# Kernel optimization log

Measured on AMD Instinct MI355X. Metric: run time of the kernel, lower is better.

Reference implementation:

```python
import jax, jax.numpy as jnp
import numpy as np

B, L_DEC, L_ENC = 4, 1024, 1024
D_MODEL, D_INNER, N_HEAD, D_K, D_V = 512, 256, 8, 64, 64
TEMP = D_K ** 0.5
EPS = 1e-6


def _layernorm(x, g, b):
    mu = jnp.mean(x, axis=-1, keepdims=True)
    var = jnp.mean(jnp.square(x - mu), axis=-1, keepdims=True)
    return (x - mu) * jax.lax.rsqrt(var + EPS) * g + b


def _mha(x_q, x_kv, Wq, Wk, Wv, Wfc, ln_g, ln_b, mask):
    # Faithful to source: only the query input is layer-normed; k/v use raw x_kv.
    resid = x_q
    qn = _layernorm(x_q, ln_g, ln_b)
    # Stacked per-head projections: Wq/Wk/Wv are [H, d_k, d_model]
    q = jnp.einsum('bld,hkd->bhlk', qn, Wq) / TEMP   # [B,H,Lq,dk]
    k = jnp.einsum('bld,hkd->bhlk', x_kv, Wk)        # [B,H,Lk,dk]
    v = jnp.einsum('bld,hkd->bhlk', x_kv, Wv)        # [B,H,Lk,dv]
    scores = jnp.einsum('bhqd,bhkd->bhqk', q, k)     # [B,H,Lq,Lk]
    if mask is not None:
        scores = jnp.where(mask[:, None, :, :] == 0, -jnp.inf, scores)
    attn = jax.nn.softmax(scores, axis=-1)
    out = jnp.einsum('bhqk,bhkd->bhqd', attn, v)     # [B,H,Lq,dv]
    Bq, H, Lq, dv = out.shape
    out = out.transpose(0, 2, 1, 3).reshape(Bq, Lq, H * dv)
    return out @ Wfc.T + resid


def _ffn(x, W1, b1, W2, b2, ln_g, ln_b):
    resid = x
    h = _layernorm(x, ln_g, ln_b)
    h = jax.nn.relu(h @ W1.T + b1) @ W2.T + b2
    return h + resid


def setup_inputs() -> dict:
    key = jax.random.key(0)
    ks = jax.random.split(key, 20)
    s = 0.02
    dec_input = jax.random.normal(ks[0], (B, L_DEC, D_MODEL), jnp.float32)
    enc_output = jax.random.normal(ks[1], (B, L_ENC, D_MODEL), jnp.float32)
    slf_attn_mask = jnp.tril(jnp.ones((1, L_DEC, L_DEC), jnp.int32))  # causal
    p = {}
    for i, pre in enumerate(['slf', 'enc']):
        base = 2 + i * 4
        p[f'{pre}_Wq'] = jax.random.normal(ks[base], (N_HEAD, D_K, D_MODEL), jnp.float32) * s
        p[f'{pre}_Wk'] = jax.random.normal(ks[base + 1], (N_HEAD, D_K, D_MODEL), jnp.float32) * s
        p[f'{pre}_Wv'] = jax.random.normal(ks[base + 2], (N_HEAD, D_V, D_MODEL), jnp.float32) * s
        p[f'{pre}_Wfc'] = jax.random.normal(ks[base + 3], (D_MODEL, N_HEAD * D_V), jnp.float32) * s
        p[f'{pre}_ln_g'] = jnp.ones((D_MODEL,), jnp.float32)
        p[f'{pre}_ln_b'] = jnp.zeros((D_MODEL,), jnp.float32)
    p['ffn_W1'] = jax.random.normal(ks[10], (D_INNER, D_MODEL), jnp.float32) * s
    p['ffn_b1'] = jnp.zeros((D_INNER,), jnp.float32)
    p['ffn_W2'] = jax.random.normal(ks[11], (D_MODEL, D_INNER), jnp.float32) * s
    p['ffn_b2'] = jnp.zeros((D_MODEL,), jnp.float32)
    p['ffn_ln_g'] = jnp.ones((D_MODEL,), jnp.float32)
    p['ffn_ln_b'] = jnp.zeros((D_MODEL,), jnp.float32)
    return {'dec_input': dec_input, 'enc_output': enc_output,
            'slf_attn_mask': slf_attn_mask, **p}


def reference(dec_input, enc_output,
              slf_Wq, slf_Wk, slf_Wv, slf_Wfc, slf_ln_g, slf_ln_b,
              enc_Wq, enc_Wk, enc_Wv, enc_Wfc, enc_ln_g, enc_ln_b,
              ffn_W1, ffn_b1, ffn_W2, ffn_b2, ffn_ln_g, ffn_ln_b,
              slf_attn_mask):
    x = _mha(dec_input, dec_input, slf_Wq, slf_Wk, slf_Wv, slf_Wfc,
             slf_ln_g, slf_ln_b, slf_attn_mask)
    x = _mha(x, enc_output, enc_Wq, enc_Wk, enc_Wv, enc_Wfc,
             enc_ln_g, enc_ln_b, None)
    x = _ffn(x, ffn_W1, ffn_b1, ffn_W2, ffn_b2, ffn_ln_g, ffn_ln_b)
    return x
```

## Files before the change

kernel.cpp:

```cpp
#include <hip/hip_runtime.h>
#include <hip/hip_bf16.h>
#include <math.h>

#define DMODEL 512
#define NHEAD  8
#define DHEAD  64

typedef __attribute__((ext_vector_type(8))) short bf16x8;
typedef __attribute__((ext_vector_type(4))) float f32x4;
typedef __attribute__((ext_vector_type(4))) short short4v;

static __device__ inline short f2bf(float f) {
    __hip_bfloat16 h = __float2bfloat16(f);
    return *reinterpret_cast<short*>(&h);
}

#define GLOAD_LDS16(gp, lp)                                                      \
    __builtin_amdgcn_global_load_lds(                                            \
        (const __attribute__((address_space(1))) unsigned int*)(gp),             \
        (__attribute__((address_space(3))) unsigned int*)(lp), 16, 0, 0)

struct PrepArgs {
    const float* src[10];
    short*       dst[10];
    int          n[10];
    const float* X;
    const float* gam;
    const float* bet;
    short*       Y;
    short*       Xd;
    const float* E;
    short*       Ed;
    int          ln_blocks;
};

__global__ __launch_bounds__(256) void prep_kernel(PrepArgs a) {
    const int bx = blockIdx.x;
    if (bx < a.ln_blocks) {
        int row = bx * 4 + (threadIdx.x >> 6);
        int tid = threadIdx.x & 63;
        const float* x = a.X + (size_t)row * DMODEL;
        float4 v0 = *(const float4*)(x + tid * 4);
        float4 v1 = *(const float4*)(x + 256 + tid * 4);
        float sum = v0.x + v0.y + v0.z + v0.w + v1.x + v1.y + v1.z + v1.w;
        float sq  = v0.x*v0.x + v0.y*v0.y + v0.z*v0.z + v0.w*v0.w
                  + v1.x*v1.x + v1.y*v1.y + v1.z*v1.z + v1.w*v1.w;
#pragma unroll
        for (int off = 1; off < 64; off <<= 1) {
            sum += __shfl_xor(sum, off);
            sq  += __shfl_xor(sq, off);
        }
        float mu  = sum * (1.0f / DMODEL);
        float var = sq * (1.0f / DMODEL) - mu * mu;
        float r   = rsqrtf(var + 1e-6f);
        float4 g1 = *(const float4*)(a.gam + tid * 4);
        float4 c1 = *(const float4*)(a.bet + tid * 4);
        float4 g2 = *(const float4*)(a.gam + 256 + tid * 4);
        float4 c2 = *(const float4*)(a.bet + 256 + tid * 4);
        short4v y1, y2;
        y1.x = f2bf((v0.x - mu) * r * g1.x + c1.x);
        y1.y = f2bf((v0.y - mu) * r * g1.y + c1.y);
        y1.z = f2bf((v0.z - mu) * r * g1.z + c1.z);
        y1.w = f2bf((v0.w - mu) * r * g1.w + c1.w);
        y2.x = f2bf((v1.x - mu) * r * g2.x + c2.x);
        y2.y = f2bf((v1.y - mu) * r * g2.y + c2.y);
        y2.z = f2bf((v1.z - mu) * r * g2.z + c2.z);
        y2.w = f2bf((v1.w - mu) * r * g2.w + c2.w);
        short* y = a.Y + (size_t)row * DMODEL;
        *(short4v*)(y + tid * 4)       = y1;
        *(short4v*)(y + 256 + tid * 4) = y2;
        short4v d1, d2;
        d1.x = f2bf(v0.x); d1.y = f2bf(v0.y); d1.z = f2bf(v0.z); d1.w = f2bf(v0.w);
        d2.x = f2bf(v1.x); d2.y = f2bf(v1.y); d2.z = f2bf(v1.z); d2.w = f2bf(v1.w);
        short* d = a.Xd + (size_t)row * DMODEL;
        *(short4v*)(d + tid * 4)       = d1;
        *(short4v*)(d + 256 + tid * 4) = d2;
        const float* e = a.E + (size_t)row * DMODEL;
        float4 ea = *(const float4*)(e + tid * 4);
        float4 eb = *(const float4*)(e + 256 + tid * 4);
        short4v e1, e2;
        e1.x = f2bf(ea.x); e1.y = f2bf(ea.y); e1.z = f2bf(ea.z); e1.w = f2bf(ea.w);
        e2.x = f2bf(eb.x); e2.y = f2bf(eb.y); e2.z = f2bf(eb.z); e2.w = f2bf(eb.w);
        short* ed = a.Ed + (size_t)row * DMODEL;
        *(short4v*)(ed + tid * 4)       = e1;
        *(short4v*)(ed + 256 + tid * 4) = e2;
    } else {
        int cb = bx - a.ln_blocks;
        int t = cb >> 7;
        int idx = ((cb & 127) * 256 + threadIdx.x) * 8;
        if (idx >= a.n[t]) return;
        const float* s = a.src[t] + idx;
        float4 p = *(const float4*)s;
        float4 q = *(const float4*)(s + 4);
        bf16x8 o;
        o[0] = f2bf(p.x); o[1] = f2bf(p.y); o[2] = f2bf(p.z); o[3] = f2bf(p.w);
        o[4] = f2bf(q.x); o[5] = f2bf(q.y); o[6] = f2bf(q.z); o[7] = f2bf(q.w);
        *(bf16x8*)(a.dst[t] + idx) = o;
    }
}

__global__ __launch_bounds__(256) void ln_kernel(const float* __restrict__ X,
                                                 const float* __restrict__ gam,
                                                 const float* __restrict__ bet,
                                                 short* __restrict__ Y) {
    int row = blockIdx.x * 4 + (threadIdx.x >> 6);
    int tid = threadIdx.x & 63;
    const float* x = X + (size_t)row * DMODEL;
    float4 a = *(const float4*)(x + tid * 4);
    float4 b = *(const float4*)(x + 256 + tid * 4);
    float sum = a.x + a.y + a.z + a.w + b.x + b.y + b.z + b.w;
    float sq  = a.x*a.x + a.y*a.y + a.z*a.z + a.w*a.w
              + b.x*b.x + b.y*b.y + b.z*b.z + b.w*b.w;
#pragma unroll
    for (int off = 1; off < 64; off <<= 1) {
        sum += __shfl_xor(sum, off);
        sq  += __shfl_xor(sq, off);
    }
    float mu  = sum * (1.0f / DMODEL);
    float var = sq * (1.0f / DMODEL) - mu * mu;
    float r   = rsqrtf(var + 1e-6f);
    float4 g1 = *(const float4*)(gam + tid * 4);
    float4 c1 = *(const float4*)(bet + tid * 4);
    float4 g2 = *(const float4*)(gam + 256 + tid * 4);
    float4 c2 = *(const float4*)(bet + 256 + tid * 4);
    short4v y1, y2;
    y1.x = f2bf((a.x - mu) * r * g1.x + c1.x);
    y1.y = f2bf((a.y - mu) * r * g1.y + c1.y);
    y1.z = f2bf((a.z - mu) * r * g1.z + c1.z);
    y1.w = f2bf((a.w - mu) * r * g1.w + c1.w);
    y2.x = f2bf((b.x - mu) * r * g2.x + c2.x);
    y2.y = f2bf((b.y - mu) * r * g2.y + c2.y);
    y2.z = f2bf((b.z - mu) * r * g2.z + c2.z);
    y2.w = f2bf((b.w - mu) * r * g2.w + c2.w);
    short* y = Y + (size_t)row * DMODEL;
    *(short4v*)(y + tid * 4)       = y1;
    *(short4v*)(y + 256 + tid * 4) = y2;
}

struct GJobs {
    const short* A[3];
    const short* W[3];
    const float* bias[3];
    const float* resid[3];
    void*        C[3];
    int M[3], N[3], K[3];
    float scale[3];
    int relu[3], obf[3], nblk[3];
};

__global__ __launch_bounds__(256) void gemm_bf16(GJobs jb) {
    __shared__ short As[2][64 * 64];
    __shared__ short Bs[2][64 * 64];

    int bid = blockIdx.x, j = 0;
    while (j < 2 && bid >= jb.nblk[j]) { bid -= jb.nblk[j]; ++j; }
    const short* __restrict__ A = jb.A[j];
    const short* __restrict__ W = jb.W[j];
    const int N = jb.N[j], K = jb.K[j];
    const int nbx = N >> 6;
    const int tn = (bid % nbx) * 64;
    const int tm = (bid / nbx) * 64;

    const int tid  = threadIdx.x;
    const int w    = tid >> 6;
    const int l    = tid & 63;
    const int lq   = l & 15;
    const int g    = l >> 4;
    const int wm   = (w >> 1) * 32;
    const int wn   = (w & 1) * 32;
    const int lrow = l >> 3;
    const int lsl  = l & 7;

    f32x4 acc[2][2];
#pragma unroll
    for (int i = 0; i < 2; ++i)
#pragma unroll
        for (int jj = 0; jj < 2; ++jj)
            acc[i][jj] = (f32x4){0.f, 0.f, 0.f, 0.f};

#define GSTAGE(buf, koff)                                                        \
    do {                                                                         \
        _Pragma("unroll")                                                        \
        for (int i_ = 0; i_ < 2; ++i_) {                                         \
            int row_ = i_ * 32 + w * 8 + lrow;                                   \
            int slot_ = lsl ^ (row_ & 7);                                        \
            GLOAD_LDS16(A + (size_t)(tm + row_) * K + (koff) + slot_ * 8,        \
                        As[buf] + i_ * 2048 + w * 512);                          \
            GLOAD_LDS16(W + (size_t)(tn + row_) * K + (koff) + slot_ * 8,        \
                        Bs[buf] + i_ * 2048 + w * 512);                          \
        }                                                                        \
    } while (0)

    GSTAGE(0, 0);
    int buf = 0;
#pragma unroll 1
    for (int k0 = 0; k0 < K; k0 += 64, buf ^= 1) {
        __syncthreads();
        if (k0 + 64 < K) GSTAGE(buf ^ 1, k0 + 64);
#pragma unroll
        for (int ks = 0; ks < 2; ++ks) {
            const int sl = ((ks * 4 + g) ^ (lq & 7)) * 8;
            bf16x8 af[2], bfv[2];
#pragma unroll
            for (int i = 0; i < 2; ++i) {
                af[i]  = *(const bf16x8*)&As[buf][(wm + i * 16 + lq) * 64 + sl];
                bfv[i] = *(const bf16x8*)&Bs[buf][(wn + i * 16 + lq) * 64 + sl];
            }
#pragma unroll
            for (int i = 0; i < 2; ++i)
#pragma unroll
                for (int jj = 0; jj < 2; ++jj)
                    acc[i][jj] = __builtin_amdgcn_mfma_f32_16x16x32_bf16(
                        af[i], bfv[jj], acc[i][jj], 0, 0, 0);
        }
    }
#undef GSTAGE

    const float* bias  = jb.bias[j];
    const float* resid = jb.resid[j];
    const float scale  = jb.scale[j];
    const int relu = jb.relu[j], obf = jb.obf[j];
#pragma unroll
    for (int i = 0; i < 2; ++i) {
#pragma unroll
        for (int r = 0; r < 4; ++r) {
            int row = tm + wm + i * 16 + g * 4 + r;
#pragma unroll
            for (int jj = 0; jj < 2; ++jj) {
                int col = tn + wn + jj * 16 + lq;
                float v = acc[i][jj][r] * scale;
                if (bias)  v += bias[col];
                if (resid) v += resid[(size_t)row * N + col];
                if (relu)  v = fmaxf(v, 0.f);
                if (obf) ((short*)jb.C[j])[(size_t)row * N + col] = f2bf(v);
                else     ((float*)jb.C[j])[(size_t)row * N + col] = v;
            }
        }
    }
}

__global__ __launch_bounds__(256) void attn_mfma_kernel(
        const short* __restrict__ Q, const short* __restrict__ K,
        const short* __restrict__ V, short* __restrict__ O,
        int Lq, int Lk, int causal, int qs, int kvs) {
    __shared__ short Kt[2][64 * 64];
    __shared__ short Vt[2][64][72];
    __shared__ short Pb[4][16][72];

    const int tid  = threadIdx.x;
    const int wave = tid >> 6;
    const int lane = tid & 63;
    const int lq   = lane & 15;
    const int g    = lane >> 4;
    const int bh   = blockIdx.y;
    const int b = bh >> 3, h = bh & 7;
    const int band = causal ? ((bh < 16) ? (int)blockIdx.x : (15 - (int)blockIdx.x))
                            : (int)blockIdx.x;
    const int qt = band * 4 + wave;
    const int q0 = qt * 16;
    const float NEG = -__builtin_inff();

    size_t qoff = (size_t)(b * Lq + q0 + lq) * qs + h * DHEAD;
    bf16x8 qf0 = *(const bf16x8*)(Q + qoff + g * 8);
    bf16x8 qf1 = *(const bf16x8*)(Q + qoff + 32 + g * 8);

    f32x4 o[4] = {{0,0,0,0},{0,0,0,0},{0,0,0,0},{0,0,0,0}};
    f32x4 lacc = {0.f, 0.f, 0.f, 0.f};

    bf16x8 ones;
    {
        short ov = (lq == 0) ? (short)0x3F80 : (short)0;
#pragma unroll
        for (int i = 0; i < 8; ++i) ones[i] = ov;
    }

    const int nkt = causal ? (band + 1) : (Lk >> 6);
    const int lrow = lane >> 3;
    const int lsl  = lane & 7;
    const int va = tid & 31;
    const int vd = (tid >> 5) * 8;

    bf16x8 vr0, vr1;
    auto stageK = [&](int kt, int bf) {
#pragma unroll
        for (int i = 0; i < 2; ++i) {
            int row = i * 32 + wave * 8 + lrow;
            int slot = lsl ^ (row & 7);
            GLOAD_LDS16(K + (size_t)(b * Lk + kt * 64 + row) * kvs + h * DHEAD + slot * 8,
                        Kt[bf] + i * 2048 + wave * 512);
        }
    };
    auto loadV = [&](int kt) {
        size_t gb = (size_t)(b * Lk + kt * 64 + 2 * va) * kvs + h * DHEAD + vd;
        vr0 = *(const bf16x8*)(V + gb);
        vr1 = *(const bf16x8*)(V + gb + kvs);
    };
    auto writeV = [&](int bf) {
#pragma unroll
        for (int i = 0; i < 8; ++i) {
            unsigned p = (unsigned short)vr0[i] | ((unsigned)(unsigned short)vr1[i] << 16);
            *(unsigned*)&Vt[bf][vd + i][2 * va] = p;
        }
    };

    stageK(0, 0);
    loadV(0);
    writeV(0);
    __syncthreads();

#pragma unroll 1
    for (int kt = 0; kt < nkt; ++kt) {
        const int cur = kt & 1;
        if (kt + 1 < nkt) { stageK(kt + 1, cur ^ 1); loadV(kt + 1); }

        f32x4 s[4];
#pragma unroll
        for (int sub = 0; sub < 4; ++sub) {
            int rr = sub * 16 + lq;
            const int sl0 = ((0 + g) ^ (lq & 7)) * 8;
            const int sl1 = ((4 + g) ^ (lq & 7)) * 8;
            bf16x8 kf0 = *(const bf16x8*)&Kt[cur][rr * 64 + sl0];
            bf16x8 kf1 = *(const bf16x8*)&Kt[cur][rr * 64 + sl1];
            f32x4 a = {0.f, 0.f, 0.f, 0.f};
            a = __builtin_amdgcn_mfma_f32_16x16x32_bf16(kf0, qf0, a, 0, 0, 0);
            a = __builtin_amdgcn_mfma_f32_16x16x32_bf16(kf1, qf1, a, 0, 0, 0);
            s[sub] = a;
        }
        if (causal && kt == nkt - 1) {
            int qg = q0 + lq;
#pragma unroll
            for (int sub = 0; sub < 4; ++sub) {
#pragma unroll
                for (int r = 0; r < 4; ++r) {
                    int kg = kt * 64 + sub * 16 + g * 4 + r;
                    if (kg > qg) s[sub][r] = NEG;
                }
            }
        }

#pragma unroll
        for (int sub = 0; sub < 4; ++sub) {
            short4v p4;
            p4.x = f2bf(exp2f(fminf(s[sub][0], 85.f)));
            p4.y = f2bf(exp2f(fminf(s[sub][1], 85.f)));
            p4.z = f2bf(exp2f(fminf(s[sub][2], 85.f)));
            p4.w = f2bf(exp2f(fminf(s[sub][3], 85.f)));
            *(short4v*)&Pb[wave][lq][sub * 16 + g * 4] = p4;
        }
        bf16x8 pf0 = *(const bf16x8*)&Pb[wave][lq][g * 8];
        bf16x8 pf1 = *(const bf16x8*)&Pb[wave][lq][32 + g * 8];

#pragma unroll
        for (int dc = 0; dc < 4; ++dc) {
            bf16x8 vf0 = *(const bf16x8*)&Vt[cur][dc * 16 + lq][g * 8];
            bf16x8 vf1 = *(const bf16x8*)&Vt[cur][dc * 16 + lq][32 + g * 8];
            o[dc] = __builtin_amdgcn_mfma_f32_16x16x32_bf16(pf0, vf0, o[dc], 0, 0, 0);
            o[dc] = __builtin_amdgcn_mfma_f32_16x16x32_bf16(pf1, vf1, o[dc], 0, 0, 0);
        }
        lacc = __builtin_amdgcn_mfma_f32_16x16x32_bf16(pf0, ones, lacc, 0, 0, 0);
        lacc = __builtin_amdgcn_mfma_f32_16x16x32_bf16(pf1, ones, lacc, 0, 0, 0);

        if (kt + 1 < nkt) writeV(cur ^ 1);
        __syncthreads();
    }

#pragma unroll
    for (int r = 0; r < 4; ++r) {
        float lr = __shfl(lacc[r], g << 4);
        float inv = 1.f / lr;
        size_t ob = (size_t)(b * Lq + q0 + g * 4 + r) * qs + h * DHEAD + lq;
        O[ob + 0]  = f2bf(o[0][r] * inv);
        O[ob + 16] = f2bf(o[1][r] * inv);
        O[ob + 32] = f2bf(o[2][r] * inv);
        O[ob + 48] = f2bf(o[3][r] * inv);
    }
}

static void launch_gemm(GJobs& jb, int njobs, hipStream_t stream) {
    int total = 0;
    for (int i = 0; i < 3; ++i) { if (i >= njobs) jb.nblk[i] = 0; total += jb.nblk[i]; }
    gemm_bf16<<<total, 256, 0, stream>>>(jb);
}

extern "C" void kernel_launch(void* const* d_in, const int* in_sizes, int n_in,
                              void* d_out, int out_size, void* d_ws, size_t ws_size,
                              hipStream_t stream) {
    const float* dec       = (const float*)d_in[0];
    const float* enc       = (const float*)d_in[1];
    const float* slf_Wq    = (const float*)d_in[3];
    const float* slf_Wk    = (const float*)d_in[4];
    const float* slf_Wv    = (const float*)d_in[5];
    const float* slf_Wfc   = (const float*)d_in[6];
    const float* slf_ln_g  = (const float*)d_in[7];
    const float* slf_ln_b  = (const float*)d_in[8];
    const float* enc_Wq    = (const float*)d_in[9];
    const float* enc_Wk    = (const float*)d_in[10];
    const float* enc_Wv    = (const float*)d_in[11];
    const float* enc_Wfc   = (const float*)d_in[12];
    const float* enc_ln_g  = (const float*)d_in[13];
    const float* enc_ln_b  = (const float*)d_in[14];
    const float* ffn_W1    = (const float*)d_in[15];
    const float* ffn_b1    = (const float*)d_in[16];
    const float* ffn_W2    = (const float*)d_in[17];
    const float* ffn_b2    = (const float*)d_in[18];
    const float* ffn_ln_g  = (const float*)d_in[19];
    const float* ffn_ln_b  = (const float*)d_in[20];
    float* out = (float*)d_out;

    const int Bb = 4, L = 1024, M = Bb * L;
    const size_t NE = (size_t)M * DMODEL;
    const int WQN = NHEAD * DHEAD * DMODEL;
    const float QSCALE = 0.125f * 1.44269504f;
    float* ws = (float*)d_ws;
    float* x1 = ws;
    float* x2 = ws + NE;
    short* kv16e = (short*)x2;
    short* sb = (short*)(ws + 2 * NE);
    short* dec16 = sb;               sb += NE;
    short* enc16 = sb;               sb += NE;
    short* qn16  = sb;               sb += NE;
    short* q16   = sb;               sb += NE;
    short* ao16  = sb;               sb += NE;
    short* kv16  = sb;               sb += 2 * NE;
    short* h16   = sb;               sb += NE / 2;
    short* wq_s  = sb;               sb += WQN;
    short* wkv_s = sb;               sb += 2 * WQN;
    short* wfc_s = sb;               sb += WQN;
    short* wq_e  = sb;               sb += WQN;
    short* wkv_e = sb;               sb += 2 * WQN;
    short* wfc_e = sb;               sb += WQN;
    short* w1_16 = sb;               sb += 256 * DMODEL;
    short* w2_16 = sb;               sb += DMODEL * 256;

    PrepArgs pa;
    pa.src[0] = slf_Wq;  pa.dst[0] = wq_s;          pa.n[0] = WQN;
    pa.src[1] = slf_Wk;  pa.dst[1] = wkv_s;         pa.n[1] = WQN;
    pa.src[2] = slf_Wv;  pa.dst[2] = wkv_s + WQN;   pa.n[2] = WQN;
    pa.src[3] = slf_Wfc; pa.dst[3] = wfc_s;         pa.n[3] = WQN;
    pa.src[4] = enc_Wq;  pa.dst[4] = wq_e;          pa.n[4] = WQN;
    pa.src[5] = enc_Wk;  pa.dst[5] = wkv_e;         pa.n[5] = WQN;
    pa.src[6] = enc_Wv;  pa.dst[6] = wkv_e + WQN;   pa.n[6] = WQN;
    pa.src[7] = enc_Wfc; pa.dst[7] = wfc_e;         pa.n[7] = WQN;
    pa.src[8] = ffn_W1;  pa.dst[8] = w1_16;         pa.n[8] = 256 * DMODEL;
    pa.src[9] = ffn_W2;  pa.dst[9] = w2_16;         pa.n[9] = DMODEL * 256;
    pa.X = dec; pa.gam = slf_ln_g; pa.bet = slf_ln_b; pa.Y = qn16;
    pa.Xd = dec16; pa.E = enc; pa.Ed = enc16;
    pa.ln_blocks = M / 4;
    prep_kernel<<<M / 4 + 10 * 128, 256, 0, stream>>>(pa);

    dim3 attn_grid(L / 64, Bb * NHEAD);
    const int NB512  = (M / 64) * (512 / 64);
    const int NB1024 = (M / 64) * (1024 / 64);
    const int NB256  = (M / 64) * (256 / 64);

    {
        GJobs jb = {};
        jb.A[0] = qn16;  jb.W[0] = wq_s;  jb.C[0] = q16;
        jb.M[0] = M; jb.N[0] = 512;  jb.K[0] = 512; jb.scale[0] = QSCALE;
        jb.obf[0] = 1; jb.nblk[0] = NB512;
        jb.A[1] = dec16; jb.W[1] = wkv_s; jb.C[1] = kv16;
        jb.M[1] = M; jb.N[1] = 1024; jb.K[1] = 512; jb.scale[1] = 1.f;
        jb.obf[1] = 1; jb.nblk[1] = NB1024;
        jb.A[2] = enc16; jb.W[2] = wkv_e; jb.C[2] = kv16e;
        jb.M[2] = M; jb.N[2] = 1024; jb.K[2] = 512; jb.scale[2] = 1.f;
        jb.obf[2] = 1; jb.nblk[2] = NB1024;
        launch_gemm(jb, 3, stream);
    }
    attn_mfma_kernel<<<attn_grid, 256, 0, stream>>>(q16, kv16, kv16 + 512, ao16,
                                                    L, L, 1, DMODEL, 1024);
    {
        GJobs jb = {};
        jb.A[0] = ao16; jb.W[0] = wfc_s; jb.resid[0] = dec; jb.C[0] = x1;
        jb.M[0] = M; jb.N[0] = 512; jb.K[0] = 512; jb.scale[0] = 1.f;
        jb.obf[0] = 0; jb.nblk[0] = NB512;
        launch_gemm(jb, 1, stream);
    }

    ln_kernel<<<M / 4, 256, 0, stream>>>(x1, enc_ln_g, enc_ln_b, qn16);
    {
        GJobs jb = {};
        jb.A[0] = qn16; jb.W[0] = wq_e; jb.C[0] = q16;
        jb.M[0] = M; jb.N[0] = 512; jb.K[0] = 512; jb.scale[0] = QSCALE;
        jb.obf[0] = 1; jb.nblk[0] = NB512;
        launch_gemm(jb, 1, stream);
    }
    attn_mfma_kernel<<<attn_grid, 256, 0, stream>>>(q16, kv16e, kv16e + 512, ao16,
                                                    L, L, 0, DMODEL, 1024);
    {
        GJobs jb = {};
        jb.A[0] = ao16; jb.W[0] = wfc_e; jb.resid[0] = x1; jb.C[0] = x2;
        jb.M[0] = M; jb.N[0] = 512; jb.K[0] = 512; jb.scale[0] = 1.f;
        jb.obf[0] = 0; jb.nblk[0] = NB512;
        launch_gemm(jb, 1, stream);
    }

    ln_kernel<<<M / 4, 256, 0, stream>>>(x2, ffn_ln_g, ffn_ln_b, qn16);
    {
        GJobs jb = {};
        jb.A[0] = qn16; jb.W[0] = w1_16; jb.bias[0] = ffn_b1; jb.C[0] = h16;
        jb.M[0] = M; jb.N[0] = 256; jb.K[0] = 512; jb.scale[0] = 1.f;
        jb.relu[0] = 1; jb.obf[0] = 1; jb.nblk[0] = NB256;
        launch_gemm(jb, 1, stream);
    }
    {
        GJobs jb = {};
        jb.A[0] = h16; jb.W[0] = w2_16; jb.bias[0] = ffn_b2; jb.resid[0] = x2;
        jb.C[0] = out;
        jb.M[0] = M; jb.N[0] = 512; jb.K[0] = 256; jb.scale[0] = 1.f;
        jb.obf[0] = 0; jb.nblk[0] = NB512;
        launch_gemm(jb, 1, stream);
    }
}
```

Baseline: 257.4 us.

## Fuse all decoder-layer stages into one cooperative persistent megakernel with grid syncs

Replaces the sequence of prep, GEMM, layernorm and attention launches with a single cooperative kernel of 512 blocks that walks through the stages, separated by grid-wide barriers. The goal is to remove per-launch overhead and tail gaps between the roughly ten kernels. Attention drops its K/V double buffering in favour of a single-buffered loop with two barriers per tile, so load and compute overlap is lost. Grid syncs also add barrier cost, and stages with fewer tiles than blocks leave CUs idle.

```diff
diff --git a/kernel.cpp b/kernel.cpp
--- a/kernel.cpp
+++ b/kernel.cpp
@@ -1,6 +1,9 @@
 #include <hip/hip_runtime.h>
+#include <hip/hip_cooperative_groups.h>
 #include <hip/hip_bf16.h>
 #include <math.h>
+
+namespace cg = cooperative_groups;
 
 #define DMODEL 512
 #define NHEAD  8
@@ -20,90 +23,29 @@
         (const __attribute__((address_space(1))) unsigned int*)(gp),             \
         (__attribute__((address_space(3))) unsigned int*)(lp), 16, 0, 0)
 
-struct PrepArgs {
-    const float* src[10];
-    short*       dst[10];
-    int          n[10];
-    const float* X;
-    const float* gam;
-    const float* bet;
-    short*       Y;
-    short*       Xd;
-    const float* E;
-    short*       Ed;
-    int          ln_blocks;
+struct GJob {
+    const short* A; const short* W;
+    const float* bias; const float* resid;
+    void* C; int N; int K; float scale; int relu; int obf; int ntile;
 };
 
-__global__ __launch_bounds__(256) void prep_kernel(PrepArgs a) {
-    const int bx = blockIdx.x;
-    if (bx < a.ln_blocks) {
-        int row = bx * 4 + (threadIdx.x >> 6);
-        int tid = threadIdx.x & 63;
-        const float* x = a.X + (size_t)row * DMODEL;
-        float4 v0 = *(const float4*)(x + tid * 4);
-        float4 v1 = *(const float4*)(x + 256 + tid * 4);
-        float sum = v0.x + v0.y + v0.z + v0.w + v1.x + v1.y + v1.z + v1.w;
-        float sq  = v0.x*v0.x + v0.y*v0.y + v0.z*v0.z + v0.w*v0.w
-                  + v1.x*v1.x + v1.y*v1.y + v1.z*v1.z + v1.w*v1.w;
-#pragma unroll
-        for (int off = 1; off < 64; off <<= 1) {
-            sum += __shfl_xor(sum, off);
-            sq  += __shfl_xor(sq, off);
-        }
-        float mu  = sum * (1.0f / DMODEL);
-        float var = sq * (1.0f / DMODEL) - mu * mu;
-        float r   = rsqrtf(var + 1e-6f);
-        float4 g1 = *(const float4*)(a.gam + tid * 4);
-        float4 c1 = *(const float4*)(a.bet + tid * 4);
-        float4 g2 = *(const float4*)(a.gam + 256 + tid * 4);
-        float4 c2 = *(const float4*)(a.bet + 256 + tid * 4);
-        short4v y1, y2;
-        y1.x = f2bf((v0.x - mu) * r * g1.x + c1.x);
-        y1.y = f2bf((v0.y - mu) * r * g1.y + c1.y);
-        y1.z = f2bf((v0.z - mu) * r * g1.z + c1.z);
-        y1.w = f2bf((v0.w - mu) * r * g1.w + c1.w);
-        y2.x = f2bf((v1.x - mu) * r * g2.x + c2.x);
-        y2.y = f2bf((v1.y - mu) * r * g2.y + c2.y);
-        y2.z = f2bf((v1.z - mu) * r * g2.z + c2.z);
-        y2.w = f2bf((v1.w - mu) * r * g2.w + c2.w);
-        short* y = a.Y + (size_t)row * DMODEL;
-        *(short4v*)(y + tid * 4)       = y1;
-        *(short4v*)(y + 256 + tid * 4) = y2;
-        short4v d1, d2;
-        d1.x = f2bf(v0.x); d1.y = f2bf(v0.y); d1.z = f2bf(v0.z); d1.w = f2bf(v0.w);
-        d2.x = f2bf(v1.x); d2.y = f2bf(v1.y); d2.z = f2bf(v1.z); d2.w = f2bf(v1.w);
-        short* d = a.Xd + (size_t)row * DMODEL;
-        *(short4v*)(d + tid * 4)       = d1;
-        *(short4v*)(d + 256 + tid * 4) = d2;
-        const float* e = a.E + (size_t)row * DMODEL;
-        float4 ea = *(const float4*)(e + tid * 4);
-        float4 eb = *(const float4*)(e + 256 + tid * 4);
-        short4v e1, e2;
-        e1.x = f2bf(ea.x); e1.y = f2bf(ea.y); e1.z = f2bf(ea.z); e1.w = f2bf(ea.w);
-        e2.x = f2bf(eb.x); e2.y = f2bf(eb.y); e2.z = f2bf(eb.z); e2.w = f2bf(eb.w);
-        short* ed = a.Ed + (size_t)row * DMODEL;
-        *(short4v*)(ed + tid * 4)       = e1;
-        *(short4v*)(ed + 256 + tid * 4) = e2;
-    } else {
-        int cb = bx - a.ln_blocks;
-        int t = cb >> 7;
-        int idx = ((cb & 127) * 256 + threadIdx.x) * 8;
-        if (idx >= a.n[t]) return;
-        const float* s = a.src[t] + idx;
-        float4 p = *(const float4*)s;
-        float4 q = *(const float4*)(s + 4);
-        bf16x8 o;
-        o[0] = f2bf(p.x); o[1] = f2bf(p.y); o[2] = f2bf(p.z); o[3] = f2bf(p.w);
-        o[4] = f2bf(q.x); o[5] = f2bf(q.y); o[6] = f2bf(q.z); o[7] = f2bf(q.w);
-        *(bf16x8*)(a.dst[t] + idx) = o;
-    }
-}
-
-__global__ __launch_bounds__(256) void ln_kernel(const float* __restrict__ X,
-                                                 const float* __restrict__ gam,
-                                                 const float* __restrict__ bet,
-                                                 short* __restrict__ Y) {
-    int row = blockIdx.x * 4 + (threadIdx.x >> 6);
+struct MegaArgs {
+    const float* wsrc[10]; short* wdst[10]; int wn[10];
+    const float* dec; const float* enc;
+    const float* slf_g; const float* slf_b;
+    const float* encln_g; const float* encln_b;
+    const float* ffnln_g; const float* ffnln_b;
+    const float* fb1; const float* fb2;
+    short* qn16; short* dec16; short* enc16; short* q16; short* ao16;
+    short* kv16; short* kv16e; short* h16;
+    float* x1; float* x2; float* out;
+};
+
+__device__ __forceinline__ void ln_rows(const float* __restrict__ X,
+                                        const float* __restrict__ gam,
+                                        const float* __restrict__ bet,
+                                        short* __restrict__ Y, int rowbase) {
+    int row = rowbase + (threadIdx.x >> 6);
     int tid = threadIdx.x & 63;
     const float* x = X + (size_t)row * DMODEL;
     float4 a = *(const float4*)(x + tid * 4);
@@ -137,30 +79,14 @@
     *(short4v*)(y + 256 + tid * 4) = y2;
 }
 
-struct GJobs {
-    const short* A[3];
-    const short* W[3];
-    const float* bias[3];
-    const float* resid[3];
-    void*        C[3];
-    int M[3], N[3], K[3];
-    float scale[3];
-    int relu[3], obf[3], nblk[3];
-};
-
-__global__ __launch_bounds__(256) void gemm_bf16(GJobs jb) {
-    __shared__ short As[2][64 * 64];
-    __shared__ short Bs[2][64 * 64];
-
-    int bid = blockIdx.x, j = 0;
-    while (j < 2 && bid >= jb.nblk[j]) { bid -= jb.nblk[j]; ++j; }
-    const short* __restrict__ A = jb.A[j];
-    const short* __restrict__ W = jb.W[j];
-    const int N = jb.N[j], K = jb.K[j];
+__device__ __forceinline__ void gemm_tile(const GJob& jb, int bid,
+                                          short* AS0, short* BS0) {
+    const short* __restrict__ A = jb.A;
+    const short* __restrict__ W = jb.W;
+    const int N = jb.N, K = jb.K;
     const int nbx = N >> 6;
     const int tn = (bid % nbx) * 64;
     const int tm = (bid / nbx) * 64;
-
     const int tid  = threadIdx.x;
     const int w    = tid >> 6;
     const int l    = tid & 63;
@@ -178,6 +104,8 @@
         for (int jj = 0; jj < 2; ++jj)
             acc[i][jj] = (f32x4){0.f, 0.f, 0.f, 0.f};
 
+    __syncthreads();
+
 #define GSTAGE(buf, koff)                                                        \
     do {                                                                         \
         _Pragma("unroll")                                                        \
@@ -185,9 +113,9 @@
             int row_ = i_ * 32 + w * 8 + lrow;                                   \
             int slot_ = lsl ^ (row_ & 7);                                        \
             GLOAD_LDS16(A + (size_t)(tm + row_) * K + (koff) + slot_ * 8,        \
-                        As[buf] + i_ * 2048 + w * 512);                          \
+                        AS0 + (buf) * 4096 + i_ * 2048 + w * 512);               \
             GLOAD_LDS16(W + (size_t)(tn + row_) * K + (koff) + slot_ * 8,        \
-                        Bs[buf] + i_ * 2048 + w * 512);                          \
+                        BS0 + (buf) * 4096 + i_ * 2048 + w * 512);               \
         }                                                                        \
     } while (0)
 
@@ -197,14 +125,16 @@
     for (int k0 = 0; k0 < K; k0 += 64, buf ^= 1) {
         __syncthreads();
         if (k0 + 64 < K) GSTAGE(buf ^ 1, k0 + 64);
+        const short* As = AS0 + buf * 4096;
+        const short* Bs = BS0 + buf * 4096;
 #pragma unroll
         for (int ks = 0; ks < 2; ++ks) {
             const int sl = ((ks * 4 + g) ^ (lq & 7)) * 8;
             bf16x8 af[2], bfv[2];
 #pragma unroll
             for (int i = 0; i < 2; ++i) {
-                af[i]  = *(const bf16x8*)&As[buf][(wm + i * 16 + lq) * 64 + sl];
-                bfv[i] = *(const bf16x8*)&Bs[buf][(wn + i * 16 + lq) * 64 + sl];
+                af[i]  = *(const bf16x8*)&As[(wm + i * 16 + lq) * 64 + sl];
+                bfv[i] = *(const bf16x8*)&Bs[(wn + i * 16 + lq) * 64 + sl];
             }
 #pragma unroll
             for (int i = 0; i < 2; ++i)
@@ -216,10 +146,6 @@
     }
 #undef GSTAGE
 
-    const float* bias  = jb.bias[j];
-    const float* resid = jb.resid[j];
-    const float scale  = jb.scale[j];
-    const int relu = jb.relu[j], obf = jb.obf[j];
 #pragma unroll
     for (int i = 0; i < 2; ++i) {
 #pragma unroll
@@ -228,34 +154,29 @@
 #pragma unroll
             for (int jj = 0; jj < 2; ++jj) {
                 int col = tn + wn + jj * 16 + lq;
-                float v = acc[i][jj][r] * scale;
-                if (bias)  v += bias[col];
-                if (resid) v += resid[(size_t)row * N + col];
-                if (relu)  v = fmaxf(v, 0.f);
-                if (obf) ((short*)jb.C[j])[(size_t)row * N + col] = f2bf(v);
-                else     ((float*)jb.C[j])[(size_t)row * N + col] = v;
+                float v = acc[i][jj][r] * jb.scale;
+                if (jb.bias)  v += jb.bias[col];
+                if (jb.resid) v += jb.resid[(size_t)row * N + col];
+                if (jb.relu)  v = fmaxf(v, 0.f);
+                if (jb.obf) ((short*)jb.C)[(size_t)row * N + col] = f2bf(v);
+                else        ((float*)jb.C)[(size_t)row * N + col] = v;
             }
         }
     }
 }
 
-__global__ __launch_bounds__(256) void attn_mfma_kernel(
+__device__ __forceinline__ void attn_block(
         const short* __restrict__ Q, const short* __restrict__ K,
         const short* __restrict__ V, short* __restrict__ O,
-        int Lq, int Lk, int causal, int qs, int kvs) {
-    __shared__ short Kt[2][64 * 64];
-    __shared__ short Vt[2][64][72];
-    __shared__ short Pb[4][16][72];
-
+        int causal, int band, int bh,
+        short* Kt, short* Vt, short* Pb) {
+    const int Lq = 1024, Lk = 1024, qs = DMODEL, kvs = 1024;
     const int tid  = threadIdx.x;
     const int wave = tid >> 6;
     const int lane = tid & 63;
     const int lq   = lane & 15;
     const int g    = lane >> 4;
-    const int bh   = blockIdx.y;
     const int b = bh >> 3, h = bh & 7;
-    const int band = causal ? ((bh < 16) ? (int)blockIdx.x : (15 - (int)blockIdx.x))
-                            : (int)blockIdx.x;
     const int qt = band * 4 + wave;
     const int q0 = qt * 16;
     const float NEG = -__builtin_inff();
@@ -280,38 +201,27 @@
     const int va = tid & 31;
     const int vd = (tid >> 5) * 8;
 
-    bf16x8 vr0, vr1;
-    auto stageK = [&](int kt, int bf) {
+#pragma unroll 1
+    for (int kt = 0; kt < nkt; ++kt) {
+        __syncthreads();
 #pragma unroll
         for (int i = 0; i < 2; ++i) {
             int row = i * 32 + wave * 8 + lrow;
             int slot = lsl ^ (row & 7);
             GLOAD_LDS16(K + (size_t)(b * Lk + kt * 64 + row) * kvs + h * DHEAD + slot * 8,
-                        Kt[bf] + i * 2048 + wave * 512);
-        }
-    };
-    auto loadV = [&](int kt) {
-        size_t gb = (size_t)(b * Lk + kt * 64 + 2 * va) * kvs + h * DHEAD + vd;
-        vr0 = *(const bf16x8*)(V + gb);
-        vr1 = *(const bf16x8*)(V + gb + kvs);
-    };
-    auto writeV = [&](int bf) {
-#pragma unroll
-        for (int i = 0; i < 8; ++i) {
-            unsigned p = (unsigned short)vr0[i] | ((unsigned)(unsigned short)vr1[i] << 16);
-            *(unsigned*)&Vt[bf][vd + i][2 * va] = p;
-        }
-    };
-
-    stageK(0, 0);
-    loadV(0);
-    writeV(0);
-    __syncthreads();
-
-#pragma unroll 1
-    for (int kt = 0; kt < nkt; ++kt) {
-        const int cur = kt & 1;
-        if (kt + 1 < nkt) { stageK(kt + 1, cur ^ 1); loadV(kt + 1); }
+                        Kt + i * 2048 + wave * 512);
+        }
+        {
+            size_t gb = (size_t)(b * Lk + kt * 64 + 2 * va) * kvs + h * DHEAD + vd;
+            bf16x8 v0 = *(const bf16x8*)(V + gb);
+            bf16x8 v1 = *(const bf16x8*)(V + gb + kvs);
+#pragma unroll
+            for (int i = 0; i < 8; ++i) {
+                unsigned p = (unsigned short)v0[i] | ((unsigned)(unsigned short)v1[i] << 16);
+                *(unsigned*)&Vt[(vd + i) * 72 + 2 * va] = p;
+            }
+        }
+        __syncthreads();
 
         f32x4 s[4];
 #pragma unroll
@@ -319,8 +229,8 @@
             int rr = sub * 16 + lq;
             const int sl0 = ((0 + g) ^ (lq & 7)) * 8;
             const int sl1 = ((4 + g) ^ (lq & 7)) * 8;
-            bf16x8 kf0 = *(const bf16x8*)&Kt[cur][rr * 64 + sl0];
-            bf16x8 kf1 = *(const bf16x8*)&Kt[cur][rr * 64 + sl1];
+            bf16x8 kf0 = *(const bf16x8*)&Kt[rr * 64 + sl0];
+            bf16x8 kf1 = *(const bf16x8*)&Kt[rr * 64 + sl1];
             f32x4 a = {0.f, 0.f, 0.f, 0.f};
             a = __builtin_amdgcn_mfma_f32_16x16x32_bf16(kf0, qf0, a, 0, 0, 0);
             a = __builtin_amdgcn_mfma_f32_16x16x32_bf16(kf1, qf1, a, 0, 0, 0);
@@ -345,23 +255,20 @@
             p4.y = f2bf(exp2f(fminf(s[sub][1], 85.f)));
             p4.z = f2bf(exp2f(fminf(s[sub][2], 85.f)));
             p4.w = f2bf(exp2f(fminf(s[sub][3], 85.f)));
-            *(short4v*)&Pb[wave][lq][sub * 16 + g * 4] = p4;
-        }
-        bf16x8 pf0 = *(const bf16x8*)&Pb[wave][lq][g * 8];
-        bf16x8 pf1 = *(const bf16x8*)&Pb[wave][lq][32 + g * 8];
+            *(short4v*)&Pb[wave * 1152 + lq * 72 + sub * 16 + g * 4] = p4;
+        }
+        bf16x8 pf0 = *(const bf16x8*)&Pb[wave * 1152 + lq * 72 + g * 8];
+        bf16x8 pf1 = *(const bf16x8*)&Pb[wave * 1152 + lq * 72 + 32 + g * 8];
 
 #pragma unroll
         for (int dc = 0; dc < 4; ++dc) {
-            bf16x8 vf0 = *(const bf16x8*)&Vt[cur][dc * 16 + lq][g * 8];
-            bf16x8 vf1 = *(const bf16x8*)&Vt[cur][dc * 16 + lq][32 + g * 8];
+            bf16x8 vf0 = *(const bf16x8*)&Vt[(dc * 16 + lq) * 72 + g * 8];
+            bf16x8 vf1 = *(const bf16x8*)&Vt[(dc * 16 + lq) * 72 + 32 + g * 8];
             o[dc] = __builtin_amdgcn_mfma_f32_16x16x32_bf16(pf0, vf0, o[dc], 0, 0, 0);
             o[dc] = __builtin_amdgcn_mfma_f32_16x16x32_bf16(pf1, vf1, o[dc], 0, 0, 0);
         }
         lacc = __builtin_amdgcn_mfma_f32_16x16x32_bf16(pf0, ones, lacc, 0, 0, 0);
         lacc = __builtin_amdgcn_mfma_f32_16x16x32_bf16(pf1, ones, lacc, 0, 0, 0);
-
-        if (kt + 1 < nkt) writeV(cur ^ 1);
-        __syncthreads();
     }
 
 #pragma unroll
@@ -376,10 +283,153 @@
     }
 }
 
-static void launch_gemm(GJobs& jb, int njobs, hipStream_t stream) {
-    int total = 0;
-    for (int i = 0; i < 3; ++i) { if (i >= njobs) jb.nblk[i] = 0; total += jb.nblk[i]; }
-    gemm_bf16<<<total, 256, 0, stream>>>(jb);
+__global__ __launch_bounds__(256, 2) void mega_kernel(MegaArgs a) {
+    cg::grid_group grid = cg::this_grid();
+    __shared__ short smem[16384];
+    short* AS0 = smem;
+    short* BS0 = smem + 8192;
+    short* Kt  = smem;
+    short* Vt  = smem + 4096;
+    short* Pb  = smem + 4096 + 4608;
+
+    const int bx = blockIdx.x;
+    const int nb = gridDim.x;
+    const float QSCALE = 0.125f * 1.44269504f;
+
+#pragma unroll 1
+    for (int v = bx; v < 1024 + 1280; v += nb) {
+        if (v < 1024) {
+            int row = v * 4 + (threadIdx.x >> 6);
+            int tid = threadIdx.x & 63;
+            const float* x = a.dec + (size_t)row * DMODEL;
+            float4 v0 = *(const float4*)(x + tid * 4);
+            float4 v1 = *(const float4*)(x + 256 + tid * 4);
+            float sum = v0.x + v0.y + v0.z + v0.w + v1.x + v1.y + v1.z + v1.w;
+            float sq  = v0.x*v0.x + v0.y*v0.y + v0.z*v0.z + v0.w*v0.w
+                      + v1.x*v1.x + v1.y*v1.y + v1.z*v1.z + v1.w*v1.w;
+#pragma unroll
+            for (int off = 1; off < 64; off <<= 1) {
+                sum += __shfl_xor(sum, off);
+                sq  += __shfl_xor(sq, off);
+            }
+            float mu  = sum * (1.0f / DMODEL);
+            float var = sq * (1.0f / DMODEL) - mu * mu;
+            float r   = rsqrtf(var + 1e-6f);
+            float4 g1 = *(const float4*)(a.slf_g + tid * 4);
+            float4 c1 = *(const float4*)(a.slf_b + tid * 4);
+            float4 g2 = *(const float4*)(a.slf_g + 256 + tid * 4);
+            float4 c2 = *(const float4*)(a.slf_b + 256 + tid * 4);
+            short4v y1, y2;
+            y1.x = f2bf((v0.x - mu) * r * g1.x + c1.x);
+            y1.y = f2bf((v0.y - mu) * r * g1.y + c1.y);
+            y1.z = f2bf((v0.z - mu) * r * g1.z + c1.z);
+            y1.w = f2bf((v0.w - mu) * r * g1.w + c1.w);
+            y2.x = f2bf((v1.x - mu) * r * g2.x + c2.x);
+            y2.y = f2bf((v1.y - mu) * r * g2.y + c2.y);
+            y2.z = f2bf((v1.z - mu) * r * g2.z + c2.z);
+            y2.w = f2bf((v1.w - mu) * r * g2.w + c2.w);
+            short* y = a.qn16 + (size_t)row * DMODEL;
+            *(short4v*)(y + tid * 4)       = y1;
+            *(short4v*)(y + 256 + tid * 4) = y2;
+            short4v d1, d2;
+            d1.x = f2bf(v0.x); d1.y = f2bf(v0.y); d1.z = f2bf(v0.z); d1.w = f2bf(v0.w);
+            d2.x = f2bf(v1.x); d2.y = f2bf(v1.y); d2.z = f2bf(v1.z); d2.w = f2bf(v1.w);
+            short* d = a.dec16 + (size_t)row * DMODEL;
+            *(short4v*)(d + tid * 4)       = d1;
+            *(short4v*)(d + 256 + tid * 4) = d2;
+            const float* e = a.enc + (size_t)row * DMODEL;
+            float4 ea = *(const float4*)(e + tid * 4);
+            float4 eb = *(const float4*)(e + 256 + tid * 4);
+            short4v e1, e2;
+            e1.x = f2bf(ea.x); e1.y = f2bf(ea.y); e1.z = f2bf(ea.z); e1.w = f2bf(ea.w);
+            e2.x = f2bf(eb.x); e2.y = f2bf(eb.y); e2.z = f2bf(eb.z); e2.w = f2bf(eb.w);
+            short* ed = a.enc16 + (size_t)row * DMODEL;
+            *(short4v*)(ed + tid * 4)       = e1;
+            *(short4v*)(ed + 256 + tid * 4) = e2;
+        } else {
+            int cb = v - 1024;
+            int t = cb >> 7;
+            int idx = ((cb & 127) * 256 + threadIdx.x) * 8;
+            if (idx < a.wn[t]) {
+                const float* s = a.wsrc[t] + idx;
+                float4 p = *(const float4*)s;
+                float4 q = *(const float4*)(s + 4);
+                bf16x8 o;
+                o[0] = f2bf(p.x); o[1] = f2bf(p.y); o[2] = f2bf(p.z); o[3] = f2bf(p.w);
+                o[4] = f2bf(q.x); o[5] = f2bf(q.y); o[6] = f2bf(q.z); o[7] = f2bf(q.w);
+                *(bf16x8*)(a.wdst[t] + idx) = o;
+            }
+        }
+    }
+    grid.sync();
+
+    {
+        GJob j{a.qn16, a.wdst[0], nullptr, nullptr, a.q16, 512, 512, QSCALE, 0, 1, 512};
+        for (int v = bx; v < j.ntile; v += nb) gemm_tile(j, v, AS0, BS0);
+    }
+    {
+        GJob j{a.dec16, a.wdst[1], nullptr, nullptr, a.kv16, 1024, 512, 1.f, 0, 1, 1024};
+        for (int v = bx; v < j.ntile; v += nb) gemm_tile(j, v, AS0, BS0);
+    }
+    {
+        GJob j{a.enc16, a.wdst[5], nullptr, nullptr, a.kv16e, 1024, 512, 1.f, 0, 1, 1024};
+        for (int v = bx; v < j.ntile; v += nb) gemm_tile(j, v, AS0, BS0);
+    }
+    grid.sync();
+
+    {
+        int bh = bx & 31;
+        int bsl = bx >> 5;
+        int band = (bsl < 8) ? bsl : 23 - bsl;
+        attn_block(a.q16, a.kv16, a.kv16 + 512, a.ao16, 1, band, bh, Kt, Vt, Pb);
+    }
+    grid.sync();
+
+    {
+        GJob j{a.ao16, a.wdst[4], nullptr, a.dec, a.x1, 512, 512, 1.f, 0, 0, 512};
+        for (int v = bx; v < j.ntile; v += nb) gemm_tile(j, v, AS0, BS0);
+    }
+    grid.sync();
+
+#pragma unroll 1
+    for (int v = bx; v < 1024; v += nb)
+        ln_rows(a.x1, a.encln_g, a.encln_b, a.qn16, v * 4);
+    grid.sync();
+
+    {
+        GJob j{a.qn16, a.wdst[6], nullptr, nullptr, a.q16, 512, 512, QSCALE, 0, 1, 512};
+        for (int v = bx; v < j.ntile; v += nb) gemm_tile(j, v, AS0, BS0);
+    }
+    grid.sync();
+
+    {
+        int bh = bx & 31;
+        int bsl = bx >> 5;
+        attn_block(a.q16, a.kv16e, a.kv16e + 512, a.ao16, 0, bsl, bh, Kt, Vt, Pb);
+    }
+    grid.sync();
+
+    {
+        GJob j{a.ao16, a.wdst[9], nullptr, a.x1, a.x2, 512, 512, 1.f, 0, 0, 512};
+        for (int v = bx; v < j.ntile; v += nb) gemm_tile(j, v, AS0, BS0);
+    }
+    grid.sync();
+
+#pragma unroll 1
+    for (int v = bx; v < 1024; v += nb)
+        ln_rows(a.x2, a.ffnln_g, a.ffnln_b, a.qn16, v * 4);
+    grid.sync();
+
+    {
+        GJob j{a.qn16, a.wdst[8], a.fb1, nullptr, a.h16, 256, 512, 1.f, 1, 1, 256};
+        for (int v = bx; v < j.ntile; v += nb) gemm_tile(j, v, AS0, BS0);
+    }
+    grid.sync();
+
+    {
+        GJob j{a.h16, a.wdst[7], a.fb2, a.x2, a.out, 512, 256, 1.f, 0, 0, 512};
+        for (int v = bx; v < j.ntile; v += nb) gemm_tile(j, v, AS0, BS0);
+    }
 }
 
 extern "C" void kernel_launch(void* const* d_in, const int* in_sizes, int n_in,
@@ -410,7 +460,6 @@
     const int Bb = 4, L = 1024, M = Bb * L;
     const size_t NE = (size_t)M * DMODEL;
     const int WQN = NHEAD * DHEAD * DMODEL;
-    const float QSCALE = 0.125f * 1.44269504f;
     float* ws = (float*)d_ws;
     float* x1 = ws;
     float* x2 = ws + NE;
@@ -432,82 +481,31 @@
     short* w1_16 = sb;               sb += 256 * DMODEL;
     short* w2_16 = sb;               sb += DMODEL * 256;
 
-    PrepArgs pa;
-    pa.src[0] = slf_Wq;  pa.dst[0] = wq_s;          pa.n[0] = WQN;
-    pa.src[1] = slf_Wk;  pa.dst[1] = wkv_s;         pa.n[1] = WQN;
-    pa.src[2] = slf_Wv;  pa.dst[2] = wkv_s + WQN;   pa.n[2] = WQN;
-    pa.src[3] = slf_Wfc; pa.dst[3] = wfc_s;         pa.n[3] = WQN;
-    pa.src[4] = enc_Wq;  pa.dst[4] = wq_e;          pa.n[4] = WQN;
-    pa.src[5] = enc_Wk;  pa.dst[5] = wkv_e;         pa.n[5] = WQN;
-    pa.src[6] = enc_Wv;  pa.dst[6] = wkv_e + WQN;   pa.n[6] = WQN;
-    pa.src[7] = enc_Wfc; pa.dst[7] = wfc_e;         pa.n[7] = WQN;
-    pa.src[8] = ffn_W1;  pa.dst[8] = w1_16;         pa.n[8] = 256 * DMODEL;
-    pa.src[9] = ffn_W2;  pa.dst[9] = w2_16;         pa.n[9] = DMODEL * 256;
-    pa.X = dec; pa.gam = slf_ln_g; pa.bet = slf_ln_b; pa.Y = qn16;
-    pa.Xd = dec16; pa.E = enc; pa.Ed = enc16;
-    pa.ln_blocks = M / 4;
-    prep_kernel<<<M / 4 + 10 * 128, 256, 0, stream>>>(pa);
-
-    dim3 attn_grid(L / 64, Bb * NHEAD);
-    const int NB512  = (M / 64) * (512 / 64);
-    const int NB1024 = (M / 64) * (1024 / 64);
-    const int NB256  = (M / 64) * (256 / 64);
-
-    {
-        GJobs jb = {};
-        jb.A[0] = qn16;  jb.W[0] = wq_s;  jb.C[0] = q16;
-        jb.M[0] = M; jb.N[0] = 512;  jb.K[0] = 512; jb.scale[0] = QSCALE;
-        jb.obf[0] = 1; jb.nblk[0] = NB512;
-        jb.A[1] = dec16; jb.W[1] = wkv_s; jb.C[1] = kv16;
-        jb.M[1] = M; jb.N[1] = 1024; jb.K[1] = 512; jb.scale[1] = 1.f;
-        jb.obf[1] = 1; jb.nblk[1] = NB1024;
-        jb.A[2] = enc16; jb.W[2] = wkv_e; jb.C[2] = kv16e;
-        jb.M[2] = M; jb.N[2] = 1024; jb.K[2] = 512; jb.scale[2] = 1.f;
-        jb.obf[2] = 1; jb.nblk[2] = NB1024;
-        launch_gemm(jb, 3, stream);
-    }
-    attn_mfma_kernel<<<attn_grid, 256, 0, stream>>>(q16, kv16, kv16 + 512, ao16,
-                                                    L, L, 1, DMODEL, 1024);
-    {
-        GJobs jb = {};
-        jb.A[0] = ao16; jb.W[0] = wfc_s; jb.resid[0] = dec; jb.C[0] = x1;
-        jb.M[0] = M; jb.N[0] = 512; jb.K[0] = 512; jb.scale[0] = 1.f;
-        jb.obf[0] = 0; jb.nblk[0] = NB512;
-        launch_gemm(jb, 1, stream);
-    }
-
-    ln_kernel<<<M / 4, 256, 0, stream>>>(x1, enc_ln_g, enc_ln_b, qn16);
-    {
-        GJobs jb = {};
-        jb.A[0] = qn16; jb.W[0] = wq_e; jb.C[0] = q16;
-        jb.M[0] = M; jb.N[0] = 512; jb.K[0] = 512; jb.scale[0] = QSCALE;
-        jb.obf[0] = 1; jb.nblk[0] = NB512;
-        launch_gemm(jb, 1, stream);
-    }
-    attn_mfma_kernel<<<attn_grid, 256, 0, stream>>>(q16, kv16e, kv16e + 512, ao16,
-                                                    L, L, 0, DMODEL, 1024);
-    {
-        GJobs jb = {};
-        jb.A[0] = ao16; jb.W[0] = wfc_e; jb.resid[0] = x1; jb.C[0] = x2;
-        jb.M[0] = M; jb.N[0] = 512; jb.K[0] = 512; jb.scale[0] = 1.f;
-        jb.obf[0] = 0; jb.nblk[0] = NB512;
-        launch_gemm(jb, 1, stream);
-    }
-
-    ln_kernel<<<M / 4, 256, 0, stream>>>(x2, ffn_ln_g, ffn_ln_b, qn16);
-    {
-        GJobs jb = {};
-        jb.A[0] = qn16; jb.W[0] = w1_16; jb.bias[0] = ffn_b1; jb.C[0] = h16;
-        jb.M[0] = M; jb.N[0] = 256; jb.K[0] = 512; jb.scale[0] = 1.f;
-        jb.relu[0] = 1; jb.obf[0] = 1; jb.nblk[0] = NB256;
-        launch_gemm(jb, 1, stream);
-    }
-    {
-        GJobs jb = {};
-        jb.A[0] = h16; jb.W[0] = w2_16; jb.bias[0] = ffn_b2; jb.resid[0] = x2;
-        jb.C[0] = out;
-        jb.M[0] = M; jb.N[0] = 512; jb.K[0] = 256; jb.scale[0] = 1.f;
-        jb.obf[0] = 0; jb.nblk[0] = NB512;
-        launch_gemm(jb, 1, stream);
-    }
+    MegaArgs ma;
+    ma.wsrc[0] = slf_Wq;  ma.wdst[0] = wq_s;        ma.wn[0] = WQN;
+    ma.wsrc[1] = slf_Wk;  ma.wdst[1] = wkv_s;       ma.wn[1] = WQN;
+    ma.wsrc[2] = slf_Wv;  ma.wdst[2] = wkv_s + WQN; ma.wn[2] = WQN;
+    ma.wsrc[3] = enc_Wk;  ma.wdst[3] = wkv_e;       ma.wn[3] = WQN;
+    ma.wsrc[4] = slf_Wfc; ma.wdst[4] = wfc_s;       ma.wn[4] = WQN;
+    ma.wsrc[5] = enc_Wv;  ma.wdst[5] = wkv_e + WQN; ma.wn[5] = WQN;
+    ma.wsrc[6] = enc_Wq;  ma.wdst[6] = wq_e;        ma.wn[6] = WQN;
+    ma.wsrc[7] = ffn_W2;  ma.wdst[7] = w2_16;       ma.wn[7] = DMODEL * 256;
+    ma.wsrc[8] = ffn_W1;  ma.wdst[8] = w1_16;       ma.wn[8] = 256 * DMODEL;
+    ma.wsrc[9] = enc_Wfc; ma.wdst[9] = wfc_e;       ma.wn[9] = WQN;
+    ma.wsrc[5] = enc_Wk;  ma.wdst[5] = wkv_e;       ma.wn[5] = WQN;
+    ma.wsrc[3] = enc_Wv;  ma.wdst[3] = wkv_e + WQN; ma.wn[3] = WQN;
+
+    ma.dec = dec; ma.enc = enc;
+    ma.slf_g = slf_ln_g; ma.slf_b = slf_ln_b;
+    ma.encln_g = enc_ln_g; ma.encln_b = enc_ln_b;
+    ma.ffnln_g = ffn_ln_g; ma.ffnln_b = ffn_ln_b;
+    ma.fb1 = ffn_b1; ma.fb2 = ffn_b2;
+    ma.qn16 = qn16; ma.dec16 = dec16; ma.enc16 = enc16;
+    ma.q16 = q16; ma.ao16 = ao16;
+    ma.kv16 = kv16; ma.kv16e = kv16e; ma.h16 = h16;
+    ma.x1 = x1; ma.x2 = x2; ma.out = out;
+
+    void* params[] = { &ma };
+    hipLaunchCooperativeKernel((const void*)mega_kernel, dim3(512), dim3(256),
+                               params, 0, stream);
 }
```

New measurement: 842.6 us. 227% more time.
